# Kernel optimization log

Hardware: AMD Instinct MI355X
Metric: run time of the kernel (lower is better)

## Reference

```python
import jax, jax.numpy as jnp
import numpy as np

B, S, D, H = 2, 2048, 1024, 16
HD = D // H  # head_dim = 64


def setup_inputs() -> dict:
    key = jax.random.key(0)
    ks = jax.random.split(key, 9)
    xav = float(np.sqrt(6.0 / (D + D)))  # xavier_uniform bound for square matrices
    def lin_w(k):
        return jax.random.uniform(k, (D, D), jnp.float32, -xav, xav)
    return {
        "x": jax.random.normal(ks[0], (B, S, D), jnp.float32),
        "mask": jnp.ones((B, S), jnp.int32),
        "Wq": lin_w(ks[1]), "bq": jnp.zeros((D,), jnp.float32),
        "Wk": lin_w(ks[2]), "bk": jnp.zeros((D,), jnp.float32),
        "Wv": lin_w(ks[3]), "bv": jnp.zeros((D,), jnp.float32),
        "Wo": lin_w(ks[4]), "bo": jnp.zeros((D,), jnp.float32),
    }


def reference(x, mask, Wq, bq, Wk, bk, Wv, bv, Wo, bo):
    # Linear projections (torch Linear: y = x @ W.T + b)
    q = x @ Wq.T + bq
    k = x @ Wk.T + bk
    v = x @ Wv.T + bv
    # [B, S, D] -> [B, H, S, HD]
    q = q.reshape(B, S, H, HD).transpose(0, 2, 1, 3)
    k = k.reshape(B, S, H, HD).transpose(0, 2, 1, 3)
    v = v.reshape(B, S, H, HD).transpose(0, 2, 1, 3)
    scores = jnp.einsum("bhqd,bhkd->bhqk", q, k) / jnp.sqrt(jnp.float32(HD))
    # mask [B, S] -> [B, 1, 1, S]; masked_fill where mask == 0
    m = mask[:, None, None, :]
    scores = jnp.where(m == 0, jnp.float32(-1e9), scores)
    attn = jax.nn.softmax(scores, axis=-1)
    # dropout in eval mode = identity
    out = jnp.einsum("bhqk,bhkd->bhqd", attn, v)
    out = out.transpose(0, 2, 1, 3).reshape(B, S, D)
    return out @ Wo.T + bo
```

## Files before the change

### kernel.cpp

```cpp
#include <hip/hip_runtime.h>
#include <stdint.h>

#define B_   2
#define S_   2048
#define D_   1024
#define H_   16
#define HD_  64
#define NTOK (B_ * S_)

typedef unsigned short u16;
typedef __bf16 bf16x8 __attribute__((ext_vector_type(8)));
typedef float  f32x4  __attribute__((ext_vector_type(4)));
typedef u16    u16x4  __attribute__((ext_vector_type(4)));

#define QSCALE 0.180336880f
#define MAXC 4.0f

#if __has_builtin(__builtin_amdgcn_exp2f)
#define EXP2(x) __builtin_amdgcn_exp2f(x)
#else
#define EXP2(x) exp2f(x)
#endif

#define OFF_FLAG ((size_t)0)
#define OFF_BIAS ((size_t)64)
#define OFF_MB   ((size_t)32768)
#define OFF_MF   ((size_t)49152)
#define OFF_X    ((size_t)65536)
#define SZ_X     ((size_t)NTOK * D_ * 2)
#define OFF_W    (OFF_X + SZ_X)
#define SZ_W     ((size_t)D_ * D_ * 2)
#define OFF_Q    (OFF_W + 4 * SZ_W)
#define SZ_T     SZ_X
#define OFF_K2   (OFF_Q + SZ_T)
#define OFF_VT   (OFF_K2 + SZ_T)
#define OFF_AO   (OFF_VT + SZ_T)

__device__ __forceinline__ float bf2f(u16 h) {
    union { uint32_t u; float f; } c; c.u = ((uint32_t)h) << 16; return c.f;
}
__device__ __forceinline__ u16 f2bf(float f) {
    union { float f; uint32_t u; } c; c.f = f;
    uint32_t r = c.u + 0x7fffu + ((c.u >> 16) & 1u);
    return (u16)(r >> 16);
}
__device__ __forceinline__ void glds16(const u16* g, u16* l) {
    __builtin_amdgcn_global_load_lds(
        (const __attribute__((address_space(1))) uint32_t*)g,
        (__attribute__((address_space(3))) uint32_t*)l,
        16, 0, 0);
}
__device__ __forceinline__ f32x4 mfma16(bf16x8 a, bf16x8 b, f32x4 c) {
    return __builtin_amdgcn_mfma_f32_16x16x32_bf16(a, b, c, 0, 0, 0);
}
__device__ __forceinline__ uint32_t pk_bf_trunc(float f0, float f1) {
    return __builtin_amdgcn_perm(__builtin_bit_cast(uint32_t, f1),
                                 __builtin_bit_cast(uint32_t, f0), 0x07060302u);
}

__global__ void convert_kernel(const void* x, const void* wq, const void* wk,
                               const void* wv, const void* wo,
                               const void* bq, const void* bk, const void* bv,
                               const void* bo, const int* mask, char* ws) {
    __shared__ int s_ok;
    const int tid = threadIdx.x;
    if (tid == 0) s_ok = 1;
    __syncthreads();
    {
        const u16* p = (const u16*)wq;
        bool bad = false;
        for (int j = 0; j < 8; ++j) {
            float v = bf2f(p[(tid * 8 + j) * 2]);
            if (!(v > -1.0f && v < 1.0f)) bad = true;
        }
        if (bad) s_ok = 0;
    }
    __syncthreads();
    const int is_bf16 = s_ok;
    if (blockIdx.x == 0 && tid == 0) *(int*)(ws + OFF_FLAG) = is_bf16;

    const uint32_t NX = (uint32_t)NTOK * D_;
    const uint32_t NW = (uint32_t)D_ * D_;
    if (!is_bf16) {
        u16* Xd = (u16*)(ws + OFF_X);
        u16* Wd = (u16*)(ws + OFF_W);
        for (uint32_t i = blockIdx.x * 256u + tid; i < NX + 4 * NW;
             i += gridDim.x * 256u) {
            const void* src; uint32_t si; u16* dst;
            if (i < NX) { src = x; si = i; dst = Xd + i; }
            else {
                uint32_t j = i - NX;
                uint32_t w = j >> 20; si = j & (NW - 1u);
                src = (w == 0) ? wq : (w == 1) ? wk : (w == 2) ? wv : wo;
                dst = Wd + j;
            }
            *dst = f2bf(((const float*)src)[si]);
        }
    }
    float* Bd = (float*)(ws + OFF_BIAS);
    float* Mbd = (float*)(ws + OFF_MB);
    int* MFd = (int*)(ws + OFF_MF);
    const uint32_t NB = 4u * D_;
    const uint32_t total2 = NB + (uint32_t)NTOK + B_ * 32;
    for (uint32_t i = blockIdx.x * 256u + tid; i < total2;
         i += gridDim.x * 256u) {
        if (i < NB) {
            uint32_t w = i >> 10; uint32_t si = i & (D_ - 1u);
            const void* src = (w == 0) ? bq : (w == 1) ? bk : (w == 2) ? bv : bo;
            Bd[i] = is_bf16 ? bf2f(((const u16*)src)[si]) : ((const float*)src)[si];
        } else if (i < NB + (uint32_t)NTOK) {
            uint32_t j = i - NB;
            Mbd[j] = (mask[j] == 0) ? -1.0e9f : 0.0f;
        } else {
            uint32_t f = i - NB - (uint32_t)NTOK;
            uint32_t bb = f >> 5, kt = f & 31;
            int any = 0;
            for (int e = 0; e < 64; ++e)
                any |= (mask[bb * S_ + kt * 64 + e] == 0);
            MFd[f] = any;
        }
    }
}

__global__ void qkv_gemm(char* ws, const void* x, const void* wq,
                         const void* wk, const void* wv) {
    __shared__ alignas(16) u16 As[128 * 32];
    __shared__ alignas(16) u16 Bs[128 * 32];
    const int z = blockIdx.z;
    const int is_bf16 = *(const int*)(ws + OFF_FLAG);
    const u16* X = is_bf16 ? (const u16*)x : (const u16*)(ws + OFF_X);
    const u16* W;
    if (is_bf16) W = (z == 0) ? (const u16*)wq : (z == 1) ? (const u16*)wk : (const u16*)wv;
    else         W = (const u16*)(ws + OFF_W + (size_t)z * SZ_W);
    const float* bias = (const float*)(ws + OFF_BIAS) + z * D_;
    u16* Qd  = (u16*)(ws + OFF_Q);
    u16* Kd  = (u16*)(ws + OFF_K2);
    u16* Vtd = (u16*)(ws + OFF_VT);

    const int tid = threadIdx.x, lane = tid & 63, wave = tid >> 6;
    const int wm = (wave & 1) * 64, wn = (wave >> 1) * 64;
    const int lr = lane & 15, quad = lane >> 4;
    const int srow = tid >> 2;
    const int scol = (((tid & 3) ^ ((tid >> 3) & 3)) * 8);
    const int rd_off = (quad ^ ((lr >> 1) & 3)) * 8;

    const u16* Araw; const u16* Braw; int m0, n0;
    if (z < 2) { Araw = W; Braw = X; m0 = blockIdx.x * 128; n0 = blockIdx.y * 128; }
    else       { Araw = X; Braw = W; m0 = blockIdx.y * 128; n0 = blockIdx.x * 128; }

    f32x4 acc[4][4];
#pragma unroll
    for (int i = 0; i < 4; i++)
#pragma unroll
        for (int j = 0; j < 4; j++) acc[i][j] = (f32x4){0.f, 0.f, 0.f, 0.f};

    const u16* Ag0 = Araw + (size_t)(m0 + srow)      * D_ + scol;
    const u16* Ag1 = Araw + (size_t)(m0 + srow + 64) * D_ + scol;
    const u16* Bg0 = Braw + (size_t)(n0 + srow)      * D_ + scol;
    const u16* Bg1 = Braw + (size_t)(n0 + srow + 64) * D_ + scol;

    for (int k0 = 0; k0 < D_; k0 += 32) {
        glds16(Ag0 + k0, &As[tid * 8]);
        glds16(Ag1 + k0, &As[2048 + tid * 8]);
        glds16(Bg0 + k0, &Bs[tid * 8]);
        glds16(Bg1 + k0, &Bs[2048 + tid * 8]);
        __syncthreads();
        bf16x8 a[4], b[4];
#pragma unroll
        for (int i = 0; i < 4; i++) a[i] = *(const bf16x8*)&As[(wm + i * 16 + lr) * 32 + rd_off];
#pragma unroll
        for (int j = 0; j < 4; j++) b[j] = *(const bf16x8*)&Bs[(wn + j * 16 + lr) * 32 + rd_off];
#pragma unroll
        for (int i = 0; i < 4; i++)
#pragma unroll
            for (int j = 0; j < 4; j++) acc[i][j] = mfma16(a[i], b[j], acc[i][j]);
        __syncthreads();
    }

    if (z < 2) {
        u16* dst0 = (z == 0) ? Qd : Kd;
        const float sc_ = (z == 0) ? QSCALE : 1.0f;
#pragma unroll
        for (int i = 0; i < 4; i++) {
            const int fb = m0 + wm + i * 16 + quad * 4;
            const f32x4 b4 = *(const f32x4*)&bias[fb];
            const int h = fb >> 6, hd0 = fb & 63;
#pragma unroll
            for (int j = 0; j < 4; j++) {
                const int tok = n0 + wn + j * 16 + lr;
                const int bb = tok >> 11, s = tok & 2047;
                u16x4 pk;
#pragma unroll
                for (int r = 0; r < 4; r++) pk[r] = f2bf((acc[i][j][r] + b4[r]) * sc_);
                *(u16x4*)&dst0[(((size_t)(bb * H_ + h)) * S_ + s) * HD_ + hd0] = pk;
            }
        }
    } else {
#pragma unroll
        for (int i = 0; i < 4; i++) {
            const int row_b = m0 + wm + i * 16 + quad * 4;
            const int bb = row_b >> 11, s0 = row_b & 2047;
#pragma unroll
            for (int j = 0; j < 4; j++) {
                const int col = n0 + wn + j * 16 + lr;
                const float bv_ = bias[col];
                const int h = col >> 6, hd = col & 63;
                u16x4 pk;
#pragma unroll
                for (int r = 0; r < 4; r++) pk[r] = f2bf(acc[i][j][r] + bv_);
                *(u16x4*)&Vtd[(((size_t)(bb * H_ + h)) * HD_ + hd) * S_ + s0] = pk;
            }
        }
    }
}

__global__ void __launch_bounds__(256)
attn_kernel(char* ws) {
    __shared__ alignas(16) char smem[49152];

    const u16* Qb  = (const u16*)(ws + OFF_Q);
    const u16* Kb  = (const u16*)(ws + OFF_K2);
    const u16* Vtb = (const u16*)(ws + OFF_VT);
    const float* Mb = (const float*)(ws + OFF_MB);
    const int* MF = (const int*)(ws + OFF_MF);
    u16* AO = (u16*)(ws + OFF_AO);

    const int tid = threadIdx.x, lane = tid & 63, wave = tid >> 6;
    const int kc = wave >> 1, qhalf = wave & 1;
    const int bh = blockIdx.y, b = bh >> 4, h = bh & 15;
    const int qb = blockIdx.x * 64 + qhalf * 32;
    const int lr = lane & 15, quad = lane >> 4;
    const int sx = lr & 7;

    const u16* Qbh = Qb  + (size_t)bh * S_ * HD_;
    const u16* Kbh = Kb  + (size_t)bh * S_ * HD_;
    const u16* Vbh = Vtb + (size_t)bh * HD_ * S_;
    const float* Mbb = Mb + b * S_;
    const int* MFb = MF + b * 32;

    u16* Ks  = (u16*)(smem + kc * 8192);
    u16* Vts = (u16*)(smem + 16384 + kc * 8192);
    u16* Pw  = (u16*)(smem + 32768 + wave * 4096);

    const int tidh = tid & 127;
    const int st_r = tidh >> 3;
    const int st_c = (tidh & 7) ^ (st_r & 7);
    const u16* Kst = Kbh + (size_t)(kc * 1024 + st_r) * HD_ + st_c * 8;
    const u16* Vst = Vbh + (size_t)st_r * S_ + kc * 1024 + st_c * 8;

    bf16x8 qf[2][2];
#pragma unroll
    for (int s = 0; s < 2; ++s)
#pragma unroll
        for (int hf = 0; hf < 2; ++hf)
            qf[s][hf] = *(const bf16x8*)&Qbh[(size_t)(qb + s * 16 + lr) * HD_ + hf * 32 + quad * 8];

    bf16x8 ones8;
#pragma unroll
    for (int i = 0; i < 8; ++i) ones8[i] = (__bf16)1.0f;

    f32x4 oacc[2][4], lacc[2];
#pragma unroll
    for (int s = 0; s < 2; ++s) {
        lacc[s] = (f32x4){0.f, 0.f, 0.f, 0.f};
#pragma unroll
        for (int j = 0; j < 4; ++j) oacc[s][j] = (f32x4){0.f, 0.f, 0.f, 0.f};
    }

    for (int it = 0; it < 16; ++it) {
        const int k0 = kc * 1024 + it * 64;
#pragma unroll
        for (int t = 0; t < 4; ++t) {
            glds16(Kst + (size_t)(it * 64 + t * 16) * HD_, &Ks[(tidh + t * 128) * 8]);
            glds16(Vst + (size_t)t * 16 * S_ + it * 64,    &Vts[(tidh + t * 128) * 8]);
        }
        __syncthreads();

        f32x4 sc[2][4];
#pragma unroll
        for (int j = 0; j < 4; ++j) {
            const int krow = (j * 16 + lr) * 64;
            bf16x8 kfA = *(const bf16x8*)&Ks[krow + ((quad    ) ^ sx) * 8];
            bf16x8 kfB = *(const bf16x8*)&Ks[krow + ((quad + 4) ^ sx) * 8];
#pragma unroll
            for (int s = 0; s < 2; ++s) {
                f32x4 t0 = mfma16(kfA, qf[s][0], (f32x4){0.f, 0.f, 0.f, 0.f});
                sc[s][j] = mfma16(kfB, qf[s][1], t0);
            }
        }
        if (MFb[kc * 16 + it]) {
#pragma unroll
            for (int j = 0; j < 4; ++j) {
                const f32x4 mb = *(const f32x4*)&Mbb[k0 + j * 16 + quad * 4];
#pragma unroll
                for (int s = 0; s < 2; ++s) sc[s][j] += mb;
            }
        }
        bf16x8 vf[4][2];
#pragma unroll
        for (int j2 = 0; j2 < 4; ++j2) {
            const int vrow = (j2 * 16 + lr) * 64;
            vf[j2][0] = *(const bf16x8*)&Vts[vrow + ((quad    ) ^ sx) * 8];
            vf[j2][1] = *(const bf16x8*)&Vts[vrow + ((quad + 4) ^ sx) * 8];
        }

#pragma unroll
        for (int s = 0; s < 2; ++s) {
            const int prow = (s * 16 + lr) * 64;
#pragma unroll
            for (int j = 0; j < 4; ++j) {
                f32x4 p;
#pragma unroll
                for (int r = 0; r < 4; ++r) p[r] = EXP2(sc[s][j][r] - MAXC);
                uint2 pk;
                pk.x = pk_bf_trunc(p[0], p[1]);
                pk.y = pk_bf_trunc(p[2], p[3]);
                *(uint2*)&Pw[prow + (((2 * j + (quad >> 1)) ^ sx) * 8) + (quad & 1) * 4] = pk;
            }
            bf16x8 pf0 = *(const bf16x8*)&Pw[prow + ((quad    ) ^ sx) * 8];
            bf16x8 pf1 = *(const bf16x8*)&Pw[prow + ((quad + 4) ^ sx) * 8];
            lacc[s] = mfma16(ones8, pf0, lacc[s]);
            lacc[s] = mfma16(ones8, pf1, lacc[s]);
#pragma unroll
            for (int j2 = 0; j2 < 4; ++j2) {
                oacc[s][j2] = mfma16(vf[j2][0], pf0, oacc[s][j2]);
                oacc[s][j2] = mfma16(vf[j2][1], pf1, oacc[s][j2]);
            }
        }
        __syncthreads();
    }

    float* Oex = (float*)smem;
    float* lex = (float*)(smem + 17408);
    if (kc == 1) {
#pragma unroll
        for (int s = 0; s < 2; ++s) {
            const int row = qhalf * 32 + s * 16 + lr;
#pragma unroll
            for (int j2 = 0; j2 < 4; ++j2)
                *(f32x4*)&Oex[row * 68 + j2 * 16 + quad * 4] = oacc[s][j2];
            if (quad == 0) lex[row] = lacc[s][0];
        }
    }
    __syncthreads();
    if (kc == 0) {
#pragma unroll
        for (int s = 0; s < 2; ++s) {
            const int row = qhalf * 32 + s * 16 + lr;
            const float linv = 1.0f / (lacc[s][0] + lex[row]);
            const int q = qb + s * 16 + lr;
            u16* dst = AO + (size_t)(b * S_ + q) * D_ + h * HD_ + quad * 4;
#pragma unroll
            for (int j2 = 0; j2 < 4; ++j2) {
                const f32x4 o2 = *(const f32x4*)&Oex[row * 68 + j2 * 16 + quad * 4];
                u16x4 pk;
#pragma unroll
                for (int r = 0; r < 4; ++r) pk[r] = f2bf((oacc[s][j2][r] + o2[r]) * linv);
                *(u16x4*)&dst[j2 * 16] = pk;
            }
        }
    }
}

__global__ void out_gemm(char* ws, const void* wo, void* dout) {
    __shared__ alignas(16) u16 As[128 * 32];
    __shared__ alignas(16) u16 Bs[64 * 32];
    const int is_bf16 = *(const int*)(ws + OFF_FLAG);
    const u16* A  = (const u16*)(ws + OFF_AO);
    const u16* Bt = is_bf16 ? (const u16*)wo : (const u16*)(ws + OFF_W + 3 * SZ_W);
    const float* bias = (const float*)(ws + OFF_BIAS) + 3 * D_;

    const int tid = threadIdx.x, lane = tid & 63, wave = tid >> 6;
    const int wm = (wave & 1) * 64, wn = (wave >> 1) * 32;
    const int m0 = blockIdx.y * 128, n0 = blockIdx.x * 64;
    const int lr = lane & 15, quad = lane >> 4;
    const int srow = tid >> 2;
    const int scol = (((tid & 3) ^ ((tid >> 3) & 3)) * 8);
    const int rd_off = (quad ^ ((lr >> 1) & 3)) * 8;

    f32x4 acc[4][2];
#pragma unroll
    for (int i = 0; i < 4; i++)
#pragma unroll
        for (int j = 0; j < 2; j++) acc[i][j] = (f32x4){0.f, 0.f, 0.f, 0.f};

    const u16* Ag0 = A  + (size_t)(m0 + srow)      * D_ + scol;
    const u16* Ag1 = A  + (size_t)(m0 + srow + 64) * D_ + scol;
    const u16* Bg0 = Bt + (size_t)(n0 + srow)      * D_ + scol;

    for (int k0 = 0; k0 < D_; k0 += 32) {
        glds16(Ag0 + k0, &As[tid * 8]);
        glds16(Ag1 + k0, &As[2048 + tid * 8]);
        glds16(Bg0 + k0, &Bs[tid * 8]);
        __syncthreads();
        bf16x8 a[4], b[2];
#pragma unroll
        for (int i = 0; i < 4; i++) a[i] = *(const bf16x8*)&As[(wm + i * 16 + lr) * 32 + rd_off];
#pragma unroll
        for (int j = 0; j < 2; j++) b[j] = *(const bf16x8*)&Bs[(wn + j * 16 + lr) * 32 + rd_off];
#pragma unroll
        for (int i = 0; i < 4; i++)
#pragma unroll
            for (int j = 0; j < 2; j++) acc[i][j] = mfma16(a[i], b[j], acc[i][j]);
        __syncthreads();
    }
#pragma unroll
    for (int i = 0; i < 4; i++) {
        const int row_b = m0 + wm + i * 16 + quad * 4;
#pragma unroll
        for (int j = 0; j < 2; j++) {
            const int col = n0 + wn + j * 16 + lr;
            const float bv_ = bias[col];
#pragma unroll
            for (int r = 0; r < 4; r++) {
                const int row = row_b + r;
                const float v = acc[i][j][r] + bv_;
                const size_t idx = (size_t)row * D_ + col;
                if (is_bf16) ((u16*)dout)[idx] = f2bf(v);
                else         ((float*)dout)[idx] = v;
            }
        }
    }
}

extern "C" void kernel_launch(void* const* d_in, const int* in_sizes, int n_in,
                              void* d_out, int out_size, void* d_ws, size_t ws_size,
                              hipStream_t stream) {
    (void)in_sizes; (void)n_in; (void)out_size; (void)ws_size;
    const void* x  = d_in[0];
    const int* mask = (const int*)d_in[1];
    const void* wq = d_in[2]; const void* bq = d_in[3];
    const void* wk = d_in[4]; const void* bk = d_in[5];
    const void* wv = d_in[6]; const void* bv = d_in[7];
    const void* wo = d_in[8]; const void* bo = d_in[9];
    char* ws = (char*)d_ws;

    convert_kernel<<<dim3(2048), dim3(256), 0, stream>>>(x, wq, wk, wv, wo,
                                                         bq, bk, bv, bo, mask, ws);
    qkv_gemm<<<dim3(8, 32, 3), dim3(256), 0, stream>>>(ws, x, wq, wk, wv);
    attn_kernel<<<dim3(S_ / 64, B_ * H_), dim3(256), 0, stream>>>(ws);
    out_gemm<<<dim3(16, 32), dim3(256), 0, stream>>>(ws, wo, d_out);
}
```

Measured before the change: 230.1 us.

## Double GEMM K-tile to 64 and give each attention wave 64 query rows

The QKV and output GEMMs now stage 64-wide K tiles with an 8-way XOR swizzle, which halves the number of barrier-separated iterations. The attention kernel now gives each wave 64 query rows instead of 32 and launches half as many blocks, so every K/V tile loaded into shared memory feeds more queries. It also shrinks the per-wave P scratch, merges score computation and exp into one loop, and sets launch_bounds to 2 blocks per unit. The EXP2 macro switches from the amdgcn builtin to exp2f. The larger per-wave state raises register pressure, and fewer attention blocks (512) could reduce occupancy or wave balance.

Result: slower. 252.3 us (+9.6%).

```diff
diff --git a/kernel.cpp b/kernel.cpp
--- a/kernel.cpp
+++ b/kernel.cpp
@@ -16,11 +16,7 @@
 #define QSCALE 0.180336880f
 #define MAXC 4.0f
 
-#if __has_builtin(__builtin_amdgcn_exp2f)
-#define EXP2(x) __builtin_amdgcn_exp2f(x)
-#else
 #define EXP2(x) exp2f(x)
-#endif
 
 #define OFF_FLAG ((size_t)0)
 #define OFF_BIAS ((size_t)64)
@@ -124,8 +120,8 @@
 
 __global__ void qkv_gemm(char* ws, const void* x, const void* wq,
                          const void* wk, const void* wv) {
-    __shared__ alignas(16) u16 As[128 * 32];
-    __shared__ alignas(16) u16 Bs[128 * 32];
+    __shared__ alignas(16) u16 As[128 * 64];
+    __shared__ alignas(16) u16 Bs[128 * 64];
     const int z = blockIdx.z;
     const int is_bf16 = *(const int*)(ws + OFF_FLAG);
     const u16* X = is_bf16 ? (const u16*)x : (const u16*)(ws + OFF_X);
@@ -140,9 +136,7 @@
     const int tid = threadIdx.x, lane = tid & 63, wave = tid >> 6;
     const int wm = (wave & 1) * 64, wn = (wave >> 1) * 64;
     const int lr = lane & 15, quad = lane >> 4;
-    const int srow = tid >> 2;
-    const int scol = (((tid & 3) ^ ((tid >> 3) & 3)) * 8);
-    const int rd_off = (quad ^ ((lr >> 1) & 3)) * 8;
+    const int sx = lr & 7;
 
     const u16* Araw; const u16* Braw; int m0, n0;
     if (z < 2) { Araw = W; Braw = X; m0 = blockIdx.x * 128; n0 = blockIdx.y * 128; }
@@ -154,26 +148,35 @@
 #pragma unroll
         for (int j = 0; j < 4; j++) acc[i][j] = (f32x4){0.f, 0.f, 0.f, 0.f};
 
-    const u16* Ag0 = Araw + (size_t)(m0 + srow)      * D_ + scol;
-    const u16* Ag1 = Araw + (size_t)(m0 + srow + 64) * D_ + scol;
-    const u16* Bg0 = Braw + (size_t)(n0 + srow)      * D_ + scol;
-    const u16* Bg1 = Braw + (size_t)(n0 + srow + 64) * D_ + scol;
-
-    for (int k0 = 0; k0 < D_; k0 += 32) {
-        glds16(Ag0 + k0, &As[tid * 8]);
-        glds16(Ag1 + k0, &As[2048 + tid * 8]);
-        glds16(Bg0 + k0, &Bs[tid * 8]);
-        glds16(Bg1 + k0, &Bs[2048 + tid * 8]);
-        __syncthreads();
-        bf16x8 a[4], b[4];
-#pragma unroll
-        for (int i = 0; i < 4; i++) a[i] = *(const bf16x8*)&As[(wm + i * 16 + lr) * 32 + rd_off];
-#pragma unroll
-        for (int j = 0; j < 4; j++) b[j] = *(const bf16x8*)&Bs[(wn + j * 16 + lr) * 32 + rd_off];
-#pragma unroll
-        for (int i = 0; i < 4; i++)
-#pragma unroll
-            for (int j = 0; j < 4; j++) acc[i][j] = mfma16(a[i], b[j], acc[i][j]);
+    const u16* Ag[4]; const u16* Bg[4];
+#pragma unroll
+    for (int t = 0; t < 4; ++t) {
+        const int c = tid + t * 256;
+        const int row = c >> 3, d = (c & 7) ^ (row & 7);
+        Ag[t] = Araw + (size_t)(m0 + row) * D_ + d * 8;
+        Bg[t] = Braw + (size_t)(n0 + row) * D_ + d * 8;
+    }
+
+    for (int k0 = 0; k0 < D_; k0 += 64) {
+#pragma unroll
+        for (int t = 0; t < 4; ++t) {
+            glds16(Ag[t] + k0, &As[(tid + t * 256) * 8]);
+            glds16(Bg[t] + k0, &Bs[(tid + t * 256) * 8]);
+        }
+        __syncthreads();
+#pragma unroll
+        for (int kh = 0; kh < 2; ++kh) {
+            const int rd = ((kh * 4 + quad) ^ sx) * 8;
+            bf16x8 a[4], b[4];
+#pragma unroll
+            for (int i = 0; i < 4; i++) a[i] = *(const bf16x8*)&As[(wm + i * 16 + lr) * 64 + rd];
+#pragma unroll
+            for (int j = 0; j < 4; j++) b[j] = *(const bf16x8*)&Bs[(wn + j * 16 + lr) * 64 + rd];
+#pragma unroll
+            for (int i = 0; i < 4; i++)
+#pragma unroll
+                for (int j = 0; j < 4; j++) acc[i][j] = mfma16(a[i], b[j], acc[i][j]);
+        }
         __syncthreads();
     }
 
@@ -214,9 +217,9 @@
     }
 }
 
-__global__ void __launch_bounds__(256)
+__global__ void __launch_bounds__(256, 2)
 attn_kernel(char* ws) {
-    __shared__ alignas(16) char smem[49152];
+    __shared__ alignas(16) char smem[40960];
 
     const u16* Qb  = (const u16*)(ws + OFF_Q);
     const u16* Kb  = (const u16*)(ws + OFF_K2);
@@ -226,9 +229,9 @@
     u16* AO = (u16*)(ws + OFF_AO);
 
     const int tid = threadIdx.x, lane = tid & 63, wave = tid >> 6;
-    const int kc = wave >> 1, qhalf = wave & 1;
+    const int kc = wave >> 1, qg = wave & 1;
     const int bh = blockIdx.y, b = bh >> 4, h = bh & 15;
-    const int qb = blockIdx.x * 64 + qhalf * 32;
+    const int qb = blockIdx.x * 128 + qg * 64;
     const int lr = lane & 15, quad = lane >> 4;
     const int sx = lr & 7;
 
@@ -240,7 +243,7 @@
 
     u16* Ks  = (u16*)(smem + kc * 8192);
     u16* Vts = (u16*)(smem + 16384 + kc * 8192);
-    u16* Pw  = (u16*)(smem + 32768 + wave * 4096);
+    u16* Pw  = (u16*)(smem + 32768 + wave * 2048);
 
     const int tidh = tid & 127;
     const int st_r = tidh >> 3;
@@ -248,9 +251,9 @@
     const u16* Kst = Kbh + (size_t)(kc * 1024 + st_r) * HD_ + st_c * 8;
     const u16* Vst = Vbh + (size_t)st_r * S_ + kc * 1024 + st_c * 8;
 
-    bf16x8 qf[2][2];
-#pragma unroll
-    for (int s = 0; s < 2; ++s)
+    bf16x8 qf[4][2];
+#pragma unroll
+    for (int s = 0; s < 4; ++s)
 #pragma unroll
         for (int hf = 0; hf < 2; ++hf)
             qf[s][hf] = *(const bf16x8*)&Qbh[(size_t)(qb + s * 16 + lr) * HD_ + hf * 32 + quad * 8];
@@ -259,9 +262,9 @@
 #pragma unroll
     for (int i = 0; i < 8; ++i) ones8[i] = (__bf16)1.0f;
 
-    f32x4 oacc[2][4], lacc[2];
-#pragma unroll
-    for (int s = 0; s < 2; ++s) {
+    f32x4 oacc[4][4], lacc[4];
+#pragma unroll
+    for (int s = 0; s < 4; ++s) {
         lacc[s] = (f32x4){0.f, 0.f, 0.f, 0.f};
 #pragma unroll
         for (int j = 0; j < 4; ++j) oacc[s][j] = (f32x4){0.f, 0.f, 0.f, 0.f};
@@ -276,42 +279,34 @@
         }
         __syncthreads();
 
-        f32x4 sc[2][4];
+        bf16x8 kf[4][2], vf[4][2];
 #pragma unroll
         for (int j = 0; j < 4; ++j) {
             const int krow = (j * 16 + lr) * 64;
-            bf16x8 kfA = *(const bf16x8*)&Ks[krow + ((quad    ) ^ sx) * 8];
-            bf16x8 kfB = *(const bf16x8*)&Ks[krow + ((quad + 4) ^ sx) * 8];
-#pragma unroll
-            for (int s = 0; s < 2; ++s) {
-                f32x4 t0 = mfma16(kfA, qf[s][0], (f32x4){0.f, 0.f, 0.f, 0.f});
-                sc[s][j] = mfma16(kfB, qf[s][1], t0);
-            }
-        }
-        if (MFb[kc * 16 + it]) {
+            kf[j][0] = *(const bf16x8*)&Ks[krow + ((quad    ) ^ sx) * 8];
+            kf[j][1] = *(const bf16x8*)&Ks[krow + ((quad + 4) ^ sx) * 8];
+            vf[j][0] = *(const bf16x8*)&Vts[krow + ((quad    ) ^ sx) * 8];
+            vf[j][1] = *(const bf16x8*)&Vts[krow + ((quad + 4) ^ sx) * 8];
+        }
+        const int masked = MFb[kc * 16 + it];
+        f32x4 mb[4];
+        if (masked) {
+#pragma unroll
+            for (int j = 0; j < 4; ++j)
+                mb[j] = *(const f32x4*)&Mbb[k0 + j * 16 + quad * 4];
+        }
+
+#pragma unroll
+        for (int s = 0; s < 4; ++s) {
+            const int prow = lr * 64;
 #pragma unroll
             for (int j = 0; j < 4; ++j) {
-                const f32x4 mb = *(const f32x4*)&Mbb[k0 + j * 16 + quad * 4];
-#pragma unroll
-                for (int s = 0; s < 2; ++s) sc[s][j] += mb;
-            }
-        }
-        bf16x8 vf[4][2];
-#pragma unroll
-        for (int j2 = 0; j2 < 4; ++j2) {
-            const int vrow = (j2 * 16 + lr) * 64;
-            vf[j2][0] = *(const bf16x8*)&Vts[vrow + ((quad    ) ^ sx) * 8];
-            vf[j2][1] = *(const bf16x8*)&Vts[vrow + ((quad + 4) ^ sx) * 8];
-        }
-
-#pragma unroll
-        for (int s = 0; s < 2; ++s) {
-            const int prow = (s * 16 + lr) * 64;
-#pragma unroll
-            for (int j = 0; j < 4; ++j) {
+                f32x4 t0 = mfma16(kf[j][0], qf[s][0], (f32x4){0.f, 0.f, 0.f, 0.f});
+                f32x4 scj = mfma16(kf[j][1], qf[s][1], t0);
+                if (masked) scj += mb[j];
                 f32x4 p;
 #pragma unroll
-                for (int r = 0; r < 4; ++r) p[r] = EXP2(sc[s][j][r] - MAXC);
+                for (int r = 0; r < 4; ++r) p[r] = EXP2(scj[r] - MAXC);
                 uint2 pk;
                 pk.x = pk_bf_trunc(p[0], p[1]);
                 pk.y = pk_bf_trunc(p[2], p[3]);
@@ -330,12 +325,12 @@
         __syncthreads();
     }
 
-    float* Oex = (float*)smem;
-    float* lex = (float*)(smem + 17408);
+    float* Oex = (float*)(smem + qg * 17664);
+    float* lex = (float*)(smem + qg * 17664 + 17408);
     if (kc == 1) {
 #pragma unroll
-        for (int s = 0; s < 2; ++s) {
-            const int row = qhalf * 32 + s * 16 + lr;
+        for (int s = 0; s < 4; ++s) {
+            const int row = s * 16 + lr;
 #pragma unroll
             for (int j2 = 0; j2 < 4; ++j2)
                 *(f32x4*)&Oex[row * 68 + j2 * 16 + quad * 4] = oacc[s][j2];
@@ -345,8 +340,8 @@
     __syncthreads();
     if (kc == 0) {
 #pragma unroll
-        for (int s = 0; s < 2; ++s) {
-            const int row = qhalf * 32 + s * 16 + lr;
+        for (int s = 0; s < 4; ++s) {
+            const int row = s * 16 + lr;
             const float linv = 1.0f / (lacc[s][0] + lex[row]);
             const int q = qb + s * 16 + lr;
             u16* dst = AO + (size_t)(b * S_ + q) * D_ + h * HD_ + quad * 4;
@@ -363,8 +358,8 @@
 }
 
 __global__ void out_gemm(char* ws, const void* wo, void* dout) {
-    __shared__ alignas(16) u16 As[128 * 32];
-    __shared__ alignas(16) u16 Bs[64 * 32];
+    __shared__ alignas(16) u16 As[128 * 64];
+    __shared__ alignas(16) u16 Bs[64 * 64];
     const int is_bf16 = *(const int*)(ws + OFF_FLAG);
     const u16* A  = (const u16*)(ws + OFF_AO);
     const u16* Bt = is_bf16 ? (const u16*)wo : (const u16*)(ws + OFF_W + 3 * SZ_W);
@@ -374,9 +369,7 @@
     const int wm = (wave & 1) * 64, wn = (wave >> 1) * 32;
     const int m0 = blockIdx.y * 128, n0 = blockIdx.x * 64;
     const int lr = lane & 15, quad = lane >> 4;
-    const int srow = tid >> 2;
-    const int scol = (((tid & 3) ^ ((tid >> 3) & 3)) * 8);
-    const int rd_off = (quad ^ ((lr >> 1) & 3)) * 8;
+    const int sx = lr & 7;
 
     f32x4 acc[4][2];
 #pragma unroll
@@ -384,24 +377,41 @@
 #pragma unroll
         for (int j = 0; j < 2; j++) acc[i][j] = (f32x4){0.f, 0.f, 0.f, 0.f};
 
-    const u16* Ag0 = A  + (size_t)(m0 + srow)      * D_ + scol;
-    const u16* Ag1 = A  + (size_t)(m0 + srow + 64) * D_ + scol;
-    const u16* Bg0 = Bt + (size_t)(n0 + srow)      * D_ + scol;
-
-    for (int k0 = 0; k0 < D_; k0 += 32) {
-        glds16(Ag0 + k0, &As[tid * 8]);
-        glds16(Ag1 + k0, &As[2048 + tid * 8]);
-        glds16(Bg0 + k0, &Bs[tid * 8]);
-        __syncthreads();
-        bf16x8 a[4], b[2];
-#pragma unroll
-        for (int i = 0; i < 4; i++) a[i] = *(const bf16x8*)&As[(wm + i * 16 + lr) * 32 + rd_off];
-#pragma unroll
-        for (int j = 0; j < 2; j++) b[j] = *(const bf16x8*)&Bs[(wn + j * 16 + lr) * 32 + rd_off];
-#pragma unroll
-        for (int i = 0; i < 4; i++)
-#pragma unroll
-            for (int j = 0; j < 2; j++) acc[i][j] = mfma16(a[i], b[j], acc[i][j]);
+    const u16* Ag[4]; const u16* Bg[2];
+#pragma unroll
+    for (int t = 0; t < 4; ++t) {
+        const int c = tid + t * 256;
+        const int row = c >> 3, d = (c & 7) ^ (row & 7);
+        Ag[t] = A + (size_t)(m0 + row) * D_ + d * 8;
+    }
+#pragma unroll
+    for (int t = 0; t < 2; ++t) {
+        const int c = tid + t * 256;
+        const int row = c >> 3, d = (c & 7) ^ (row & 7);
+        Bg[t] = Bt + (size_t)(n0 + row) * D_ + d * 8;
+    }
+
+    for (int k0 = 0; k0 < D_; k0 += 64) {
+#pragma unroll
+        for (int t = 0; t < 4; ++t)
+            glds16(Ag[t] + k0, &As[(tid + t * 256) * 8]);
+#pragma unroll
+        for (int t = 0; t < 2; ++t)
+            glds16(Bg[t] + k0, &Bs[(tid + t * 256) * 8]);
+        __syncthreads();
+#pragma unroll
+        for (int kh = 0; kh < 2; ++kh) {
+            const int rd = ((kh * 4 + quad) ^ sx) * 8;
+            bf16x8 a[4], b[2];
+#pragma unroll
+            for (int i = 0; i < 4; i++) a[i] = *(const bf16x8*)&As[(wm + i * 16 + lr) * 64 + rd];
+#pragma unroll
+            for (int j = 0; j < 2; j++) b[j] = *(const bf16x8*)&Bs[(wn + j * 16 + lr) * 64 + rd];
+#pragma unroll
+            for (int i = 0; i < 4; i++)
+#pragma unroll
+                for (int j = 0; j < 2; j++) acc[i][j] = mfma16(a[i], b[j], acc[i][j]);
+        }
         __syncthreads();
     }
 #pragma unroll
@@ -438,6 +448,6 @@
     convert_kernel<<<dim3(2048), dim3(256), 0, stream>>>(x, wq, wk, wv, wo,
                                                          bq, bk, bv, bo, mask, ws);
     qkv_gemm<<<dim3(8, 32, 3), dim3(256), 0, stream>>>(ws, x, wq, wk, wv);
-    attn_kernel<<<dim3(S_ / 64, B_ * H_), dim3(256), 0, stream>>>(ws);
+    attn_kernel<<<dim3(S_ / 128, B_ * H_), dim3(256), 0, stream>>>(ws);
     out_gemm<<<dim3(16, 32), dim3(256), 0, stream>>>(ws, wo, d_out);
 }
```
